# Kernel optimization log

Measured on AMD Instinct MI355X. Metric: run time of the kernel, lower is better.

The kernel has to match this reference:

```python
import jax, jax.numpy as jnp
import numpy as np

DIM = 1024
D_STATE = 16
D_CONV = 4
EXPAND = 2
D_INNER = DIM * EXPAND
DT_RANK = 64  # ceil(1024/16)
N_EXP = 8
TOP_K = 2
HID = DIM * 2
B, T = 2, 2048
EPS = 1e-5


def setup_inputs() -> dict:
    key = jax.random.key(0)
    ks = jax.random.split(key, 16)
    s = 0.02
    # dt bias init (softplus-inverse of dt in [1e-3, 1e-1]) as in the torch code
    dt_init = jnp.exp(jax.random.uniform(ks[0], (D_INNER,)) * (np.log(0.1) - np.log(0.001)) + np.log(0.001))
    dt_proj_b = dt_init + jnp.log(-jnp.expm1(-dt_init))
    A_log = jnp.broadcast_to(jnp.log(jnp.arange(1, D_STATE + 1, dtype=jnp.float32))[None, :], (D_INNER, D_STATE))
    return {
        "x": jax.random.normal(ks[1], (B, T, DIM), jnp.float32),
        "ssm_state": jnp.zeros((B, D_INNER, D_STATE), jnp.float32),
        "conv_state": jnp.zeros((B, D_INNER, D_CONV - 1), jnp.float32),
        "ln1_s": jnp.ones((DIM,), jnp.float32), "ln1_b": jnp.zeros((DIM,), jnp.float32),
        "ln2_s": jnp.ones((DIM,), jnp.float32), "ln2_b": jnp.zeros((DIM,), jnp.float32),
        "in_proj_w": jax.random.normal(ks[2], (2 * D_INNER, DIM), jnp.float32) * s,
        "conv_w": jax.random.normal(ks[3], (D_INNER, 1, D_CONV), jnp.float32) * 0.2,
        "conv_b": jnp.zeros((D_INNER,), jnp.float32),
        "x_proj_w": jax.random.normal(ks[4], (DT_RANK + 2 * D_STATE, D_INNER), jnp.float32) * s,
        "dt_proj_w": jax.random.normal(ks[5], (D_INNER, DT_RANK), jnp.float32) * s,
        "dt_proj_b": dt_proj_b,
        "A_log": A_log,
        "Dp": jnp.ones((D_INNER,), jnp.float32),
        "out_proj_w": jax.random.normal(ks[6], (DIM, D_INNER), jnp.float32) * s,
        "router_w": jax.random.normal(ks[7], (N_EXP, DIM), jnp.float32) * s,
        "w_gate": jax.random.normal(ks[8], (N_EXP, HID, DIM), jnp.float32) * s,
        "w_up": jax.random.normal(ks[9], (N_EXP, HID, DIM), jnp.float32) * s,
        "w_down": jax.random.normal(ks[10], (N_EXP, DIM, HID), jnp.float32) * s,
    }


def _layernorm(x, scale, bias):
    mu = x.mean(-1, keepdims=True)
    var = ((x - mu) ** 2).mean(-1, keepdims=True)
    return (x - mu) * jax.lax.rsqrt(var + EPS) * scale + bias


def _mamba(xn, ssm_state, conv_state, in_proj_w, conv_w, conv_b, x_proj_w, dt_proj_w, dt_proj_b, A_log, Dp, out_proj_w):
    xz = jnp.einsum("btd,ed->bte", xn, in_proj_w)          # [B,T,2*di]
    x_in, z = xz[..., :D_INNER], xz[..., D_INNER:]
    # causal depthwise conv with running buffer
    xc = jnp.concatenate([conv_state, x_in.transpose(0, 2, 1)], axis=2)  # [B,di,T+dc-1]
    new_conv_state = xc[:, :, -(D_CONV - 1):]
    conv = jax.lax.conv_general_dilated(xc, conv_w, (1,), "VALID",
                                        dimension_numbers=("NCH", "OIH", "NCH"),
                                        feature_group_count=D_INNER)
    conv = conv + conv_b[None, :, None]
    xcs = jax.nn.silu(conv).transpose(0, 2, 1)              # [B,T,di]
    proj = jnp.einsum("bti,pi->btp", xcs, x_proj_w)
    dt_raw = proj[..., :DT_RANK]
    Bp = proj[..., DT_RANK:DT_RANK + D_STATE]
    Cp = proj[..., DT_RANK + D_STATE:]
    dt = jax.nn.softplus(jnp.einsum("btr,ir->bti", dt_raw, dt_proj_w) + dt_proj_b)
    A = -jnp.exp(A_log)                                     # [di,ds]

    def step(h, inp):
        dt_t, B_t, C_t, x_t = inp                           # [B,di],[B,ds],[B,ds],[B,di]
        dA = jnp.exp(dt_t[..., None] * A)                   # [B,di,ds]
        dB = dt_t[..., None] * B_t[:, None, :]
        h = dA * h + dB * x_t[..., None]
        y = jnp.sum(h * C_t[:, None, :], -1) + Dp * x_t
        return h, y

    xs = (dt.transpose(1, 0, 2), Bp.transpose(1, 0, 2), Cp.transpose(1, 0, 2), xcs.transpose(1, 0, 2))
    h, ys = jax.lax.scan(step, ssm_state, xs)
    y = ys.transpose(1, 0, 2) * jax.nn.silu(z)
    out = jnp.einsum("bti,di->btd", y, out_proj_w)
    return out, h, new_conv_state


def _moe(x, router_w, w_gate, w_up, w_down):
    Bb, Tt, D = x.shape
    xf = x.reshape(-1, D)                                   # [N,D]
    probs = jax.nn.softmax(xf @ router_w.T, axis=-1)        # [N,E]
    tw, ti = jax.lax.top_k(probs, TOP_K)
    tw = tw / tw.sum(-1, keepdims=True)
    gate = jax.nn.silu(jnp.einsum("nd,ehd->neh", xf, w_gate))
    up = jnp.einsum("nd,ehd->neh", xf, w_up)
    eo = jnp.einsum("neh,edh->ned", gate * up, w_down)      # [N,E,D]
    sel = jnp.take_along_axis(eo, ti[:, :, None], axis=1)   # [N,K,D]
    out = (tw[..., None] * sel).sum(1)
    return out.reshape(Bb, Tt, D)


def reference(x, ssm_state, conv_state, ln1_s, ln1_b, ln2_s, ln2_b, in_proj_w, conv_w, conv_b,
              x_proj_w, dt_proj_w, dt_proj_b, A_log, Dp, out_proj_w, router_w, w_gate, w_up, w_down):
    mamba_out, h, new_conv = _mamba(_layernorm(x, ln1_s, ln1_b), ssm_state, conv_state,
                                    in_proj_w, conv_w, conv_b, x_proj_w, dt_proj_w, dt_proj_b,
                                    A_log, Dp, out_proj_w)
    x1 = x + mamba_out
    out = x1 + _moe(_layernorm(x1, ln2_s, ln2_b), router_w, w_gate, w_up, w_down)
    return out
```

## Files before the change

### kernel.cpp

```cpp
#include <hip/hip_runtime.h>
#include <hip/hip_bf16.h>
#include <math.h>

#define DIM 1024
#define D_STATE 16
#define D_CONV 4
#define D_INNER 2048
#define DT_RANK 64
#define N_EXP 8
#define TOP_K 2
#define HID 2048
#define BB 2
#define TT 2048
#define NTOK (BB*TT)
#define NSLOT (NTOK*TOP_K)
#define EPS 1e-5f
#define NCHUNK 64
#define CLEN (TT/NCHUNK)
#define XPJ_KS 8
#define XPJ_KLEN (D_INNER/XPJ_KS)

#define OFF_R0   ((size_t)0)
#define OFF_R1   ((size_t)4194304)
#define OFF_R2   ((size_t)8388608)
#define OFF_XZ   ((size_t)10485760)
#define OFF_H    OFF_XZ
#define OFF_WU   ((size_t)18874368)
#define OFF_XCS  ((size_t)27262976)
#define OFF_DTP  ((size_t)35651584)
#define OFF_X1   ((size_t)44040192)
#define OFF_PROJ ((size_t)48234496)
#define OFF_TW   ((size_t)48627712)
#define OFF_INT  ((size_t)48635904)
#define OFF_XPW  ((size_t)48668672)
#define IO_TI    0
#define IO_CNT   8192
#define IO_CUR   8200
#define IO_OFS   8208
#define IO_TOK   8216
#define IO_SLOT  16408

typedef __attribute__((ext_vector_type(4))) float f32x4;
typedef __attribute__((ext_vector_type(8))) __bf16 bf16x8;
typedef __attribute__((ext_vector_type(4))) __bf16 bf16x4;

__device__ __forceinline__ float siluf(float v){ return v / (1.f + expf(-v)); }

__device__ __forceinline__ f32x4 mfma16(bf16x8 a, bf16x8 b, f32x4 c){
    return __builtin_amdgcn_mfma_f32_16x16x32_bf16(a, b, c, 0, 0, 0);
}

__device__ __forceinline__ void gload16(const void* g, void* l){
    __builtin_amdgcn_global_load_lds(
        (const __attribute__((address_space(1))) unsigned int*)g,
        (__attribute__((address_space(3))) unsigned int*)l, 16, 0, 0);
}

__device__ __forceinline__ void cvt_store16(__bf16* dst, f32x4 a0, f32x4 a1, f32x4 a2, f32x4 a3){
    bf16x8 p0, p1;
    #pragma unroll
    for (int j = 0; j < 4; ++j){
        p0[j]   = (__bf16)a0[j];
        p0[j+4] = (__bf16)a1[j];
        p1[j]   = (__bf16)a2[j];
        p1[j+4] = (__bf16)a3[j];
    }
    *(bf16x8*)dst = p0;
    *(bf16x8*)(dst+8) = p1;
}

__global__ __launch_bounds__(256) void cvt_w_kernel(const float* __restrict__ src,
    __bf16* __restrict__ dst, int n4)
{
    int i = blockIdx.x*256 + threadIdx.x;
    int stride = gridDim.x*256;
    for (; i < n4; i += stride){
        f32x4 v = *(const f32x4*)(src + (size_t)i*4);
        bf16x4 o;
        o[0] = (__bf16)v[0]; o[1] = (__bf16)v[1];
        o[2] = (__bf16)v[2]; o[3] = (__bf16)v[3];
        *(bf16x4*)(dst + (size_t)i*4) = o;
    }
}

__global__ __launch_bounds__(256) void cvt_pad_xproj(const float* __restrict__ src,
    __bf16* __restrict__ dst)
{
    int i = blockIdx.x*256 + threadIdx.x;
    int base = i*4;
    int row = base >> 11;
    bf16x4 o;
    if (row < 96){
        f32x4 v = *(const f32x4*)(src + base);
        o[0] = (__bf16)v[0]; o[1] = (__bf16)v[1];
        o[2] = (__bf16)v[2]; o[3] = (__bf16)v[3];
    } else {
        o[0] = (__bf16)0.f; o[1] = (__bf16)0.f;
        o[2] = (__bf16)0.f; o[3] = (__bf16)0.f;
    }
    *(bf16x4*)(dst + base) = o;
}

__global__ __launch_bounds__(256) void ln_kernel(const float* __restrict__ x,
    const float* __restrict__ s, const float* __restrict__ b,
    __bf16* __restrict__ obf)
{
    int t = blockIdx.x;
    const float* xp = x + (size_t)t * DIM;
    float v[4]; float sum = 0.f, sq = 0.f;
    #pragma unroll
    for (int j = 0; j < 4; ++j){
        v[j] = xp[threadIdx.x + 256*j];
        sum += v[j]; sq += v[j]*v[j];
    }
    #pragma unroll
    for (int off = 32; off; off >>= 1){
        sum += __shfl_xor(sum, off, 64);
        sq  += __shfl_xor(sq , off, 64);
    }
    __shared__ float red[4][2];
    int w = threadIdx.x >> 6, lane = threadIdx.x & 63;
    if (lane == 0){ red[w][0] = sum; red[w][1] = sq; }
    __syncthreads();
    sum = red[0][0]+red[1][0]+red[2][0]+red[3][0];
    sq  = red[0][1]+red[1][1]+red[2][1]+red[3][1];
    float mu = sum * (1.f/DIM);
    float var = sq * (1.f/DIM) - mu*mu;
    float r = rsqrtf(var + EPS);
    #pragma unroll
    for (int j = 0; j < 4; ++j){
        int d = threadIdx.x + 256*j;
        obf[(size_t)t*DIM + d] = (__bf16)((v[j]-mu)*r*s[d] + b[d]);
    }
}

__global__ __launch_bounds__(256) void ln2_router_kernel(const float* __restrict__ x,
    const float* __restrict__ s, const float* __restrict__ b,
    const float* __restrict__ rw, __bf16* __restrict__ obf,
    float* __restrict__ tw, int* __restrict__ ti, int* __restrict__ counts)
{
    int t = blockIdx.x;
    const float* xp = x + (size_t)t * DIM;
    float v[4]; float sum = 0.f, sq = 0.f;
    #pragma unroll
    for (int j = 0; j < 4; ++j){
        v[j] = xp[threadIdx.x + 256*j];
        sum += v[j]; sq += v[j]*v[j];
    }
    #pragma unroll
    for (int off = 32; off; off >>= 1){
        sum += __shfl_xor(sum, off, 64);
        sq  += __shfl_xor(sq , off, 64);
    }
    __shared__ float red[4][2];
    __shared__ float red2[4][N_EXP];
    int w = threadIdx.x >> 6, lane = threadIdx.x & 63;
    if (lane == 0){ red[w][0] = sum; red[w][1] = sq; }
    __syncthreads();
    sum = red[0][0]+red[1][0]+red[2][0]+red[3][0];
    sq  = red[0][1]+red[1][1]+red[2][1]+red[3][1];
    float mu = sum * (1.f/DIM);
    float var = sq * (1.f/DIM) - mu*mu;
    float r = rsqrtf(var + EPS);
    float p[N_EXP] = {};
    #pragma unroll
    for (int j = 0; j < 4; ++j){
        int d = threadIdx.x + 256*j;
        float o = (v[j]-mu)*r*s[d] + b[d];
        obf[(size_t)t*DIM + d] = (__bf16)o;
        #pragma unroll
        for (int e = 0; e < N_EXP; ++e) p[e] += o * rw[e*DIM + d];
    }
    #pragma unroll
    for (int e = 0; e < N_EXP; ++e){
        #pragma unroll
        for (int off = 32; off; off >>= 1) p[e] += __shfl_xor(p[e], off, 64);
    }
    if (lane == 0){
        #pragma unroll
        for (int e = 0; e < N_EXP; ++e) red2[w][e] = p[e];
    }
    __syncthreads();
    if (threadIdx.x == 0){
        float q[N_EXP];
        #pragma unroll
        for (int e = 0; e < N_EXP; ++e)
            q[e] = red2[0][e]+red2[1][e]+red2[2][e]+red2[3][e];
        float mx = q[0];
        #pragma unroll
        for (int e = 1; e < N_EXP; ++e) mx = fmaxf(mx, q[e]);
        float ssum = 0.f;
        #pragma unroll
        for (int e = 0; e < N_EXP; ++e){ q[e] = expf(q[e]-mx); ssum += q[e]; }
        int i0 = 0;
        #pragma unroll
        for (int e = 1; e < N_EXP; ++e) if (q[e] > q[i0]) i0 = e;
        int i1 = (i0 == 0) ? 1 : 0;
        #pragma unroll
        for (int e = 0; e < N_EXP; ++e) if (e != i0 && q[e] > q[i1]) i1 = e;
        float w0 = q[i0]/ssum, w1 = q[i1]/ssum;
        float sw = w0 + w1; w0 /= sw; w1 /= sw;
        tw[t*2] = w0; tw[t*2+1] = w1;
        ti[t*2] = i0; ti[t*2+1] = i1;
        atomicAdd(&counts[i0], 1);
        atomicAdd(&counts[i1], 1);
    }
}

template<int MODE, int EPI, int CBF, int SWZ>
__global__ __launch_bounds__(256,3) void mfma_gemm_fast(
    const __bf16* __restrict__ A, const __bf16* __restrict__ W,
    const void* __restrict__ RG, void* __restrict__ Cv,
    const int* __restrict__ tok_of_slot, const int* __restrict__ counts,
    const int* __restrict__ offs, int M, int N, int K, int lda)
{
    int bx = blockIdx.x, by = blockIdx.y;
    if (SWZ){
        int nwg = gridDim.x*gridDim.y;
        int id = by*gridDim.x + bx;
        int swz = (id & 7)*(nwg >> 3) + (id >> 3);
        bx = swz % gridDim.x; by = swz / gridDim.x;
    }
    int e    = (MODE == 0) ? 0 : blockIdx.z;
    int cnt  = (MODE == 0) ? M : counts[e];
    int base = (MODE == 0) ? 0 : offs[e];
    int m0 = by * 128;
    if (m0 >= cnt) return;
    int n0 = bx * 128;
    const __bf16* We = W + (size_t)e * N * K;

    __shared__ __bf16 As[3*128*32];
    __shared__ __bf16 Ws[3*128*32];

    int tid = threadIdx.x;
    int wave = tid >> 6, lane = tid & 63;
    int c0 = wave*2, c1 = wave*2 + 1;
    int lr0 = c0*16 + (lane >> 2);
    int lr1 = c1*16 + (lane >> 2);
    int koff = (((lane & 3) ^ ((lane >> 3) & 3)) * 8);

    int ar0, ar1;
    {
        int m0c = m0 + lr0, m1c = m0 + lr1;
        if (MODE != 0){
            if (m0c >= cnt) m0c = cnt - 1;
            if (m1c >= cnt) m1c = cnt - 1;
        }
        if (MODE == 1){ ar0 = tok_of_slot[base + m0c]; ar1 = tok_of_slot[base + m1c]; }
        else if (MODE == 2){ ar0 = base + m0c; ar1 = base + m1c; }
        else { ar0 = m0c; ar1 = m1c; }
    }
    const __bf16* aS0 = A + (size_t)ar0 * lda + koff;
    const __bf16* aS1 = A + (size_t)ar1 * lda + koff;
    const __bf16* wS0 = We + (size_t)(n0 + lr0) * K + koff;
    const __bf16* wS1 = We + (size_t)(n0 + lr1) * K + koff;
    __bf16* ldsA0 = As + c0*512;
    __bf16* ldsA1 = As + c1*512;
    __bf16* ldsW0 = Ws + c0*512;
    __bf16* ldsW1 = Ws + c1*512;

    int wm = (wave >> 1) * 64, wn = (wave & 1) * 64;
    int fr = lane & 15;
    const int scb = (((lane >> 4) ^ ((lane >> 1) & 3)) * 8);

    f32x4 acc[4][4];
    #pragma unroll
    for (int i = 0; i < 4; ++i)
        #pragma unroll
        for (int j = 0; j < 4; ++j)
            acc[i][j] = (f32x4){0.f, 0.f, 0.f, 0.f};

    int NK = K >> 5;
    gload16(aS0, ldsA0);        gload16(aS1, ldsA1);
    gload16(wS0, ldsW0);        gload16(wS1, ldsW1);
    if (NK > 1){
        gload16(aS0 + 32, ldsA0 + 4096); gload16(aS1 + 32, ldsA1 + 4096);
        gload16(wS0 + 32, ldsW0 + 4096); gload16(wS1 + 32, ldsW1 + 4096);
    }

    int cur = 0;
    for (int t = 0; t < NK; ++t){
        if (t + 2 < NK){
            int nb = cur + 2; if (nb >= 3) nb -= 3;
            int off = nb*4096;
            size_t ko = (size_t)(t+2)*32;
            gload16(aS0 + ko, ldsA0 + off);
            gload16(aS1 + ko, ldsA1 + off);
            gload16(wS0 + ko, ldsW0 + off);
            gload16(wS1 + ko, ldsW1 + off);
            asm volatile("s_waitcnt vmcnt(8)" ::: "memory");
        } else if (t + 1 < NK){
            asm volatile("s_waitcnt vmcnt(4)" ::: "memory");
        } else {
            asm volatile("s_waitcnt vmcnt(0)" ::: "memory");
        }
        __builtin_amdgcn_s_barrier();
        int bo = cur*4096;
        bf16x8 af[4], bf[4];
        #pragma unroll
        for (int i = 0; i < 4; ++i)
            af[i] = *(const bf16x8*)&As[bo + (wm + i*16 + fr)*32 + scb];
        #pragma unroll
        for (int j = 0; j < 4; ++j)
            bf[j] = *(const bf16x8*)&Ws[bo + (wn + j*16 + fr)*32 + scb];
        __builtin_amdgcn_s_setprio(1);
        #pragma unroll
        for (int i = 0; i < 4; ++i)
            #pragma unroll
            for (int j = 0; j < 4; ++j)
                acc[i][j] = mfma16(af[i], bf[j], acc[i][j]);
        __builtin_amdgcn_s_setprio(0);
        __builtin_amdgcn_s_barrier();
        cur = cur + 1; if (cur >= 3) cur -= 3;
    }

    int orow = (lane >> 4) * 4;
    int ocol = lane & 15;
    #pragma unroll
    for (int i = 0; i < 4; ++i){
        #pragma unroll
        for (int jj = 0; jj < 4; ++jj){
            #pragma unroll
            for (int j = 0; j < 4; ++j){
                int m = m0 + wm + i*16 + orow + j;
                int n = n0 + wn + jj*16 + ocol;
                if (m < cnt){
                    size_t row = (size_t)(base + m);
                    float v = acc[i][jj][j];
                    if (EPI == 1) v += ((const float*)RG)[row * (size_t)N + n];
                    if (CBF) ((__bf16*)Cv)[row * (size_t)N + n] = (__bf16)v;
                    else     ((float* )Cv)[row * (size_t)N + n] = v;
                }
            }
        }
    }
}

__global__ __launch_bounds__(256,2) void moe_gateup_fast(
    const __bf16* __restrict__ A, const __bf16* __restrict__ Wg,
    const __bf16* __restrict__ Wu, const int* __restrict__ tok_of_slot,
    const int* __restrict__ counts, const int* __restrict__ offs,
    __bf16* __restrict__ H)
{
    int e = blockIdx.z;
    int cnt = counts[e];
    int base = offs[e];
    int m0 = blockIdx.y * 128;
    if (m0 >= cnt) return;
    int n0 = blockIdx.x * 128;
    const __bf16* Wge = Wg + (size_t)e * HID * DIM;
    const __bf16* Wue = Wu + (size_t)e * HID * DIM;

    __shared__ __bf16 As[3*128*32];
    __shared__ __bf16 Gs[3*128*32];
    __shared__ __bf16 Us[3*128*32];

    int tid = threadIdx.x;
    int wave = tid >> 6, lane = tid & 63;
    int c0 = wave*2, c1 = wave*2 + 1;
    int lr0 = c0*16 + (lane >> 2);
    int lr1 = c1*16 + (lane >> 2);
    int koff = (((lane & 3) ^ ((lane >> 3) & 3)) * 8);

    int m0c = m0 + lr0, m1c = m0 + lr1;
    if (m0c >= cnt) m0c = cnt - 1;
    if (m1c >= cnt) m1c = cnt - 1;
    int ar0 = tok_of_slot[base + m0c];
    int ar1 = tok_of_slot[base + m1c];

    const __bf16* aS0 = A + (size_t)ar0 * DIM + koff;
    const __bf16* aS1 = A + (size_t)ar1 * DIM + koff;
    const __bf16* gS0 = Wge + (size_t)(n0 + lr0) * DIM + koff;
    const __bf16* gS1 = Wge + (size_t)(n0 + lr1) * DIM + koff;
    const __bf16* uS0 = Wue + (size_t)(n0 + lr0) * DIM + koff;
    const __bf16* uS1 = Wue + (size_t)(n0 + lr1) * DIM + koff;
    __bf16* ldsA0 = As + c0*512;
    __bf16* ldsA1 = As + c1*512;
    __bf16* ldsG0 = Gs + c0*512;
    __bf16* ldsG1 = Gs + c1*512;
    __bf16* ldsU0 = Us + c0*512;
    __bf16* ldsU1 = Us + c1*512;

    int wm = (wave >> 1) * 64, wn = (wave & 1) * 64;
    int fr = lane & 15;
    const int scb = (((lane >> 4) ^ ((lane >> 1) & 3)) * 8);

    f32x4 accg[4][4], accu[4][4];
    #pragma unroll
    for (int i = 0; i < 4; ++i)
        #pragma unroll
        for (int j = 0; j < 4; ++j){
            accg[i][j] = (f32x4){0.f, 0.f, 0.f, 0.f};
            accu[i][j] = (f32x4){0.f, 0.f, 0.f, 0.f};
        }

    gload16(aS0, ldsA0); gload16(aS1, ldsA1);
    gload16(gS0, ldsG0); gload16(gS1, ldsG1);
    gload16(uS0, ldsU0); gload16(uS1, ldsU1);
    gload16(aS0 + 32, ldsA0 + 4096); gload16(aS1 + 32, ldsA1 + 4096);
    gload16(gS0 + 32, ldsG0 + 4096); gload16(gS1 + 32, ldsG1 + 4096);
    gload16(uS0 + 32, ldsU0 + 4096); gload16(uS1 + 32, ldsU1 + 4096);

    const int NK = DIM >> 5;
    int cur = 0;
    for (int t = 0; t < NK; ++t){
        if (t + 2 < NK){
            int nb = cur + 2; if (nb >= 3) nb -= 3;
            int off = nb*4096;
            size_t ko = (size_t)(t+2)*32;
            gload16(aS0 + ko, ldsA0 + off);
            gload16(aS1 + ko, ldsA1 + off);
            gload16(gS0 + ko, ldsG0 + off);
            gload16(gS1 + ko, ldsG1 + off);
            gload16(uS0 + ko, ldsU0 + off);
            gload16(uS1 + ko, ldsU1 + off);
            asm volatile("s_waitcnt vmcnt(12)" ::: "memory");
        } else if (t + 1 < NK){
            asm volatile("s_waitcnt vmcnt(6)" ::: "memory");
        } else {
            asm volatile("s_waitcnt vmcnt(0)" ::: "memory");
        }
        __builtin_amdgcn_s_barrier();
        int bo = cur*4096;
        bf16x8 af[4], gf[4], uf[4];
        #pragma unroll
        for (int i = 0; i < 4; ++i){
            af[i] = *(const bf16x8*)&As[bo + (wm + i*16 + fr)*32 + scb];
            gf[i] = *(const bf16x8*)&Gs[bo + (wn + i*16 + fr)*32 + scb];
            uf[i] = *(const bf16x8*)&Us[bo + (wn + i*16 + fr)*32 + scb];
        }
        __builtin_amdgcn_s_setprio(1);
        #pragma unroll
        for (int i = 0; i < 4; ++i)
            #pragma unroll
            for (int j = 0; j < 4; ++j){
                accg[i][j] = mfma16(af[i], gf[j], accg[i][j]);
                accu[i][j] = mfma16(af[i], uf[j], accu[i][j]);
            }
        __builtin_amdgcn_s_setprio(0);
        __builtin_amdgcn_s_barrier();
        cur = cur + 1; if (cur >= 3) cur -= 3;
    }

    int orow = (lane >> 4) * 4;
    int ocol = lane & 15;
    #pragma unroll
    for (int i = 0; i < 4; ++i){
        #pragma unroll
        for (int jj = 0; jj < 4; ++jj){
            #pragma unroll
            for (int j = 0; j < 4; ++j){
                int m = m0 + wm + i*16 + orow + j;
                if (m < cnt){
                    int n = n0 + wn + jj*16 + ocol;
                    size_t row = (size_t)(base + m);
                    float g = accg[i][jj][j], u = accu[i][jj][j];
                    H[row * (size_t)HID + n] = (__bf16)(siluf(g) * u);
                }
            }
        }
    }
}

__global__ __launch_bounds__(256,3) void xproj_ks_kernel(
    const __bf16* __restrict__ A, const __bf16* __restrict__ W,
    float* __restrict__ Cpart)
{
    int m0 = blockIdx.y * 128;
    int kbeg = blockIdx.z * XPJ_KLEN;

    __shared__ __bf16 As[3*128*32];
    __shared__ __bf16 Ws[3*128*32];

    int tid = threadIdx.x;
    int wave = tid >> 6, lane = tid & 63;
    int c0 = wave*2, c1 = wave*2 + 1;
    int lr0 = c0*16 + (lane >> 2);
    int lr1 = c1*16 + (lane >> 2);
    int koff = (((lane & 3) ^ ((lane >> 3) & 3)) * 8);

    const __bf16* aS0 = A + (size_t)(m0 + lr0) * D_INNER + kbeg + koff;
    const __bf16* aS1 = A + (size_t)(m0 + lr1) * D_INNER + kbeg + koff;
    const __bf16* wS0 = W + (size_t)lr0 * D_INNER + kbeg + koff;
    const __bf16* wS1 = W + (size_t)lr1 * D_INNER + kbeg + koff;
    __bf16* ldsA0 = As + c0*512;
    __bf16* ldsA1 = As + c1*512;
    __bf16* ldsW0 = Ws + c0*512;
    __bf16* ldsW1 = Ws + c1*512;

    int wm = (wave >> 1) * 64, wn = (wave & 1) * 64;
    int fr = lane & 15;
    const int scb = (((lane >> 4) ^ ((lane >> 1) & 3)) * 8);

    f32x4 acc[4][4];
    #pragma unroll
    for (int i = 0; i < 4; ++i)
        #pragma unroll
        for (int j = 0; j < 4; ++j)
            acc[i][j] = (f32x4){0.f, 0.f, 0.f, 0.f};

    gload16(aS0, ldsA0); gload16(aS1, ldsA1);
    gload16(wS0, ldsW0); gload16(wS1, ldsW1);
    gload16(aS0 + 32, ldsA0 + 4096); gload16(aS1 + 32, ldsA1 + 4096);
    gload16(wS0 + 32, ldsW0 + 4096); gload16(wS1 + 32, ldsW1 + 4096);

    const int NK = XPJ_KLEN >> 5;
    int cur = 0;
    for (int t = 0; t < NK; ++t){
        if (t + 2 < NK){
            int nb = cur + 2; if (nb >= 3) nb -= 3;
            int off = nb*4096;
            size_t ko = (size_t)(t+2)*32;
            gload16(aS0 + ko, ldsA0 + off);
            gload16(aS1 + ko, ldsA1 + off);
            gload16(wS0 + ko, ldsW0 + off);
            gload16(wS1 + ko, ldsW1 + off);
            asm volatile("s_waitcnt vmcnt(8)" ::: "memory");
        } else if (t + 1 < NK){
            asm volatile("s_waitcnt vmcnt(4)" ::: "memory");
        } else {
            asm volatile("s_waitcnt vmcnt(0)" ::: "memory");
        }
        __builtin_amdgcn_s_barrier();
        int bo = cur*4096;
        bf16x8 af[4], bf[4];
        #pragma unroll
        for (int i = 0; i < 4; ++i)
            af[i] = *(const bf16x8*)&As[bo + (wm + i*16 + fr)*32 + scb];
        #pragma unroll
        for (int j = 0; j < 4; ++j)
            bf[j] = *(const bf16x8*)&Ws[bo + (wn + j*16 + fr)*32 + scb];
        __builtin_amdgcn_s_setprio(1);
        #pragma unroll
        for (int i = 0; i < 4; ++i)
            #pragma unroll
            for (int j = 0; j < 4; ++j)
                acc[i][j] = mfma16(af[i], bf[j], acc[i][j]);
        __builtin_amdgcn_s_setprio(0);
        __builtin_amdgcn_s_barrier();
        cur = cur + 1; if (cur >= 3) cur -= 3;
    }

    float* Cz = Cpart + (size_t)blockIdx.z * NTOK * 128;
    int orow = (lane >> 4) * 4;
    int ocol = lane & 15;
    #pragma unroll
    for (int i = 0; i < 4; ++i){
        #pragma unroll
        for (int jj = 0; jj < 4; ++jj){
            #pragma unroll
            for (int j = 0; j < 4; ++j){
                int m = m0 + wm + i*16 + orow + j;
                int n = wn + jj*16 + ocol;
                Cz[(size_t)m * 128 + n] = acc[i][jj][j];
            }
        }
    }
}

__global__ __launch_bounds__(256) void xproj_reduce(const float* __restrict__ Cpart,
    float* __restrict__ proj)
{
    int idx = blockIdx.x*256 + threadIdx.x;
    int t = idx / 96, n = idx - t*96;
    float s = 0.f;
    #pragma unroll
    for (int z = 0; z < XPJ_KS; ++z)
        s += Cpart[(size_t)z * NTOK * 128 + (size_t)t * 128 + n];
    proj[idx] = s;
}

__global__ __launch_bounds__(256,2) void dt_gemm(
    const float* __restrict__ A, const float* __restrict__ W,
    const float* __restrict__ bias, float* __restrict__ C,
    int M, int N, int K, int lda)
{
    int m0 = blockIdx.y * 128;
    int n0 = blockIdx.x * 128;

    __shared__ __bf16 As[128*32];
    __shared__ __bf16 Ws[128*32];

    int tid = threadIdx.x;
    int srow = tid >> 1;
    int scol = (tid & 1) * 16;

    const float* af = A + (size_t)(m0 + srow) * lda + scol;
    const float* wptr = W + (size_t)(n0 + srow) * K + scol;

    f32x4 raf[4], rw[4];
    #pragma unroll
    for (int q = 0; q < 4; ++q){
        raf[q] = *(const f32x4*)(af + q*4);
        rw[q]  = *(const f32x4*)(wptr + q*4);
    }

    int wave = tid >> 6, lane = tid & 63;
    int wm = (wave >> 1) * 64, wn = (wave & 1) * 64;
    int fr = lane & 15, fk = (lane >> 4) * 8;

    f32x4 acc[4][4];
    #pragma unroll
    for (int i = 0; i < 4; ++i)
        #pragma unroll
        for (int j = 0; j < 4; ++j)
            acc[i][j] = (f32x4){0.f, 0.f, 0.f, 0.f};

    for (int k0 = 0; k0 < K; k0 += 32){
        cvt_store16(&As[srow*32 + scol], raf[0], raf[1], raf[2], raf[3]);
        cvt_store16(&Ws[srow*32 + scol], rw[0], rw[1], rw[2], rw[3]);
        __syncthreads();
        if (k0 + 32 < K){
            #pragma unroll
            for (int q = 0; q < 4; ++q){
                raf[q] = *(const f32x4*)(af + k0 + 32 + q*4);
                rw[q]  = *(const f32x4*)(wptr + k0 + 32 + q*4);
            }
        }
        bf16x8 afr[4], bfr[4];
        #pragma unroll
        for (int i = 0; i < 4; ++i)
            afr[i] = *(const bf16x8*)&As[(wm + i*16 + fr)*32 + fk];
        #pragma unroll
        for (int i = 0; i < 4; ++i)
            bfr[i] = *(const bf16x8*)&Ws[(wn + i*16 + fr)*32 + fk];
        #pragma unroll
        for (int i = 0; i < 4; ++i)
            #pragma unroll
            for (int j = 0; j < 4; ++j)
                acc[i][j] = mfma16(afr[i], bfr[j], acc[i][j]);
        __syncthreads();
    }

    int orow = (lane >> 4) * 4;
    int ocol = lane & 15;
    #pragma unroll
    for (int i = 0; i < 4; ++i){
        #pragma unroll
        for (int jj = 0; jj < 4; ++jj){
            #pragma unroll
            for (int j = 0; j < 4; ++j){
                int m = m0 + wm + i*16 + orow + j;
                int n = n0 + wn + jj*16 + ocol;
                if (m < M && n < N){
                    float v = acc[i][jj][j] + bias[n];
                    v = (v > 20.f) ? v : log1pf(expf(v));
                    C[(size_t)m * N + n] = v;
                }
            }
        }
    }
}

__global__ __launch_bounds__(256) void conv_kernel(const float* __restrict__ xz,
    const float* __restrict__ cs, const float* __restrict__ cw,
    const float* __restrict__ cb, float* __restrict__ xcs,
    __bf16* __restrict__ xcs_bf)
{
    int idx = blockIdx.x*256 + threadIdx.x;
    int d = idx & (D_INNER-1);
    int bt = idx >> 11;
    int b = bt >> 11;
    int t = bt & (TT-1);
    float acc = cb[d];
    #pragma unroll
    for (int k = 0; k < 4; ++k){
        int tau = t + k - 3;
        float xv;
        if (tau >= 0) xv = xz[(size_t)(b*TT + tau)*(2*D_INNER) + d];
        else          xv = cs[((size_t)b*D_INNER + d)*3 + (tau + 3)];
        acc += cw[d*4 + k] * xv;
    }
    float v = siluf(acc);
    xcs[idx] = v;
    xcs_bf[idx] = (__bf16)v;
}

__global__ __launch_bounds__(256) void scan_pass1(const float* __restrict__ dtp,
    const float* __restrict__ proj, const float* __restrict__ xcs,
    const float* __restrict__ A_log, float* __restrict__ hend,
    float* __restrict__ sumdt)
{
    int gid = blockIdx.x*256 + threadIdx.x;
    int bd = gid & (BB*D_INNER-1);
    int chunk = gid >> 12;
    int b = bd >> 11, d = bd & (D_INNER-1);
    float As[D_STATE], h[D_STATE];
    #pragma unroll
    for (int s = 0; s < D_STATE; ++s){
        As[s] = -__expf(A_log[d*D_STATE + s]);
        h[s] = 0.f;
    }
    float sdt = 0.f;
    int base = b*TT + chunk*CLEN;
    for (int t = 0; t < CLEN; ++t){
        size_t bt = (size_t)(base + t);
        float dt = dtp[bt*D_INNER + d];
        float x  = xcs[bt*D_INNER + d];
        f32x4 Bv[4];
        #pragma unroll
        for (int q = 0; q < 4; ++q) Bv[q] = *(const f32x4*)(proj + bt*96 + DT_RANK + q*4);
        float dtx = dt * x;
        sdt += dt;
        #pragma unroll
        for (int s = 0; s < D_STATE; ++s)
            h[s] = __expf(dt*As[s])*h[s] + Bv[s>>2][s&3]*dtx;
    }
    size_t hb = ((size_t)bd*NCHUNK + chunk)*D_STATE;
    #pragma unroll
    for (int q = 0; q < 4; ++q)
        *(f32x4*)(hend + hb + q*4) = (f32x4){h[q*4], h[q*4+1], h[q*4+2], h[q*4+3]};
    sumdt[bd*NCHUNK + chunk] = sdt;
}

__global__ __launch_bounds__(256) void scan_combine(const float* __restrict__ hend,
    const float* __restrict__ sumdt, const float* __restrict__ A_log,
    const float* __restrict__ ssm0, float* __restrict__ hstart)
{
    int gid = blockIdx.x*256 + threadIdx.x;
    int s = gid & 15;
    int bd = gid >> 4;
    int b = bd >> 11, d = bd & (D_INNER-1);
    float As = -__expf(A_log[d*D_STATE + s]);
    float h = ssm0[((size_t)b*D_INNER + d)*D_STATE + s];
    for (int c = 0; c < NCHUNK; ++c){
        size_t idx = ((size_t)bd*NCHUNK + c)*D_STATE + s;
        hstart[idx] = h;
        h = hend[idx] + __expf(As * sumdt[bd*NCHUNK + c]) * h;
    }
}

__global__ __launch_bounds__(256) void scan_pass3(const float* __restrict__ dtp,
    const float* __restrict__ proj, const float* __restrict__ xcs,
    const float* __restrict__ xz, const float* __restrict__ A_log,
    const float* __restrict__ Dp, const float* __restrict__ hstart,
    __bf16* __restrict__ ym)
{
    int gid = blockIdx.x*256 + threadIdx.x;
    int bd = gid & (BB*D_INNER-1);
    int chunk = gid >> 12;
    int b = bd >> 11, d = bd & (D_INNER-1);
    float As[D_STATE], h[D_STATE];
    #pragma unroll
    for (int s = 0; s < D_STATE; ++s)
        As[s] = -__expf(A_log[d*D_STATE + s]);
    size_t hb = ((size_t)bd*NCHUNK + chunk)*D_STATE;
    #pragma unroll
    for (int q = 0; q < 4; ++q){
        f32x4 hv = *(const f32x4*)(hstart + hb + q*4);
        h[q*4] = hv[0]; h[q*4+1] = hv[1]; h[q*4+2] = hv[2]; h[q*4+3] = hv[3];
    }
    float Dd = Dp[d];
    int base = b*TT + chunk*CLEN;
    for (int t = 0; t < CLEN; ++t){
        size_t bt = (size_t)(base + t);
        float dt = dtp[bt*D_INNER + d];
        float x  = xcs[bt*D_INNER + d];
        f32x4 Bv[4], Cv[4];
        #pragma unroll
        for (int q = 0; q < 4; ++q){
            Bv[q] = *(const f32x4*)(proj + bt*96 + DT_RANK + q*4);
            Cv[q] = *(const f32x4*)(proj + bt*96 + DT_RANK + D_STATE + q*4);
        }
        float dtx = dt * x;
        float p = 0.f;
        #pragma unroll
        for (int s = 0; s < D_STATE; ++s){
            h[s] = __expf(dt*As[s])*h[s] + Bv[s>>2][s&3]*dtx;
            p += h[s] * Cv[s>>2][s&3];
        }
        float y = p + Dd*x;
        float z = xz[bt*(2*D_INNER) + D_INNER + d];
        float sz = z / (1.f + __expf(-z));
        ym[bt*D_INNER + d] = (__bf16)(y * sz);
    }
}

__global__ void offs_kernel(const int* __restrict__ counts, int* __restrict__ offs)
{
    if (threadIdx.x == 0 && blockIdx.x == 0){
        int s = 0;
        for (int e = 0; e < N_EXP; ++e){ offs[e] = s; s += counts[e]; }
    }
}

__global__ __launch_bounds__(256) void assign_kernel(const int* __restrict__ ti,
    const int* __restrict__ offs, int* __restrict__ cursors,
    int* __restrict__ tok_of_slot, int* __restrict__ slot_of)
{
    int t = blockIdx.x*256 + threadIdx.x;
    if (t >= NTOK) return;
    #pragma unroll
    for (int k = 0; k < TOP_K; ++k){
        int e = ti[t*2 + k];
        int pos = atomicAdd(&cursors[e], 1);
        int slot = offs[e] + pos;
        tok_of_slot[slot] = t;
        slot_of[t*2 + k] = slot;
    }
}

__global__ __launch_bounds__(256) void final_kernel(const float* __restrict__ x1,
    const float* __restrict__ down_out, const float* __restrict__ tw,
    const int* __restrict__ slot_of, float* __restrict__ out)
{
    int idx4 = blockIdx.x*256 + threadIdx.x;
    int t = idx4 >> 8;
    int c = idx4 & 255;
    float w0 = tw[t*2], w1 = tw[t*2+1];
    size_t s0 = (size_t)slot_of[t*2] * DIM;
    size_t s1 = (size_t)slot_of[t*2+1] * DIM;
    float4 a = *(const float4*)(x1 + (size_t)t*DIM + c*4);
    float4 d0 = *(const float4*)(down_out + s0 + c*4);
    float4 d1 = *(const float4*)(down_out + s1 + c*4);
    float4 r;
    r.x = a.x + w0*d0.x + w1*d1.x;
    r.y = a.y + w0*d0.y + w1*d1.y;
    r.z = a.z + w0*d0.z + w1*d1.z;
    r.w = a.w + w0*d0.w + w1*d1.w;
    *(float4*)(out + (size_t)t*DIM + c*4) = r;
}

extern "C" void kernel_launch(void* const* d_in, const int* in_sizes, int n_in,
                              void* d_out, int out_size, void* d_ws, size_t ws_size,
                              hipStream_t stream)
{
    const float* x        = (const float*)d_in[0];
    const float* ssm0     = (const float*)d_in[1];
    const float* conv0    = (const float*)d_in[2];
    const float* ln1_s    = (const float*)d_in[3];
    const float* ln1_b    = (const float*)d_in[4];
    const float* ln2_s    = (const float*)d_in[5];
    const float* ln2_b    = (const float*)d_in[6];
    const float* in_proj  = (const float*)d_in[7];
    const float* conv_w   = (const float*)d_in[8];
    const float* conv_b   = (const float*)d_in[9];
    const float* x_proj   = (const float*)d_in[10];
    const float* dt_proj  = (const float*)d_in[11];
    const float* dt_b     = (const float*)d_in[12];
    const float* A_log    = (const float*)d_in[13];
    const float* Dp       = (const float*)d_in[14];
    const float* out_proj = (const float*)d_in[15];
    const float* router_w = (const float*)d_in[16];
    const float* w_gate   = (const float*)d_in[17];
    const float* w_up     = (const float*)d_in[18];
    const float* w_down   = (const float*)d_in[19];
    float* out = (float*)d_out;

    float* ws = (float*)d_ws;
    __bf16* xn_bf  = (__bf16*)(ws + OFF_R0);
    float*  hend   = ws + OFF_R0;
    __bf16* ym_bf  = (__bf16*)(ws + OFF_R0);
    float*  xpart  = ws + OFF_R1;
    float*  hst    = ws + OFF_R1;
    float*  sdt    = ws + OFF_R2;
    __bf16* opbf   = (__bf16*)(ws + OFF_R2);
    __bf16* xn2bf  = (__bf16*)(ws + OFF_R2);
    float*  xz     = ws + OFF_XZ;
    __bf16* H      = (__bf16*)(ws + OFF_H);
    __bf16* wubf   = (__bf16*)(ws + OFF_WU);
    float*  xcs    = ws + OFF_XCS;
    float*  dnout  = ws + OFF_XCS;
    float*  dtp    = ws + OFF_DTP;
    __bf16* ipbf   = (__bf16*)(ws + OFF_DTP);
    __bf16* wgbf   = (__bf16*)(ws + OFF_DTP);
    __bf16* wdbf   = (__bf16*)(ws + OFF_DTP);
    __bf16* xcs_bf = (__bf16*)(ws + OFF_X1);
    float*  x1     = ws + OFF_X1;
    float*  proj   = ws + OFF_PROJ;
    float*  tw     = ws + OFF_TW;
    __bf16* xpw    = (__bf16*)(ws + OFF_XPW);
    int*    ip     = (int*)(ws + OFF_INT);
    int* ti          = ip + IO_TI;
    int* counts      = ip + IO_CNT;
    int* cursors     = ip + IO_CUR;
    int* offs        = ip + IO_OFS;
    int* tok_of_slot = ip + IO_TOK;
    int* slot_of     = ip + IO_SLOT;

    hipMemsetAsync(counts, 0, 16*sizeof(int), stream);

    cvt_w_kernel<<<1024, 256, 0, stream>>>(in_proj, ipbf, (2*D_INNER*DIM)/4);
    ln_kernel<<<NTOK, 256, 0, stream>>>(x, ln1_s, ln1_b, xn_bf);
    mfma_gemm_fast<0,0,0,1><<<dim3(32,32), 256, 0, stream>>>(xn_bf, ipbf, nullptr, xz,
        nullptr, nullptr, nullptr, NTOK, 2*D_INNER, DIM, DIM);
    conv_kernel<<<(NTOK*D_INNER)/256, 256, 0, stream>>>(xz, conv0, conv_w, conv_b, xcs, xcs_bf);
    cvt_pad_xproj<<<256, 256, 0, stream>>>(x_proj, xpw);
    xproj_ks_kernel<<<dim3(1,32,XPJ_KS), 256, 0, stream>>>(xcs_bf, xpw, xpart);
    xproj_reduce<<<(NTOK*96)/256, 256, 0, stream>>>(xpart, proj);
    dt_gemm<<<dim3(16,32), 256, 0, stream>>>(proj, dt_proj, dt_b, dtp,
        NTOK, D_INNER, DT_RANK, 96);
    scan_pass1<<<1024, 256, 0, stream>>>(dtp, proj, xcs, A_log, hend, sdt);
    scan_combine<<<256, 256, 0, stream>>>(hend, sdt, A_log, ssm0, hst);
    scan_pass3<<<1024, 256, 0, stream>>>(dtp, proj, xcs, xz, A_log, Dp, hst, ym_bf);
    cvt_w_kernel<<<512, 256, 0, stream>>>(out_proj, opbf, (DIM*D_INNER)/4);
    mfma_gemm_fast<0,1,0,1><<<dim3(8,32), 256, 0, stream>>>(ym_bf, opbf, x, x1,
        nullptr, nullptr, nullptr, NTOK, DIM, D_INNER, D_INNER);
    ln2_router_kernel<<<NTOK, 256, 0, stream>>>(x1, ln2_s, ln2_b, router_w,
        xn2bf, tw, ti, counts);
    offs_kernel<<<1, 64, 0, stream>>>(counts, offs);
    assign_kernel<<<NTOK/256, 256, 0, stream>>>(ti, offs, cursors, tok_of_slot, slot_of);
    cvt_w_kernel<<<2048, 256, 0, stream>>>(w_gate, wgbf, (N_EXP*HID*DIM)/4);
    cvt_w_kernel<<<2048, 256, 0, stream>>>(w_up, wubf, (N_EXP*HID*DIM)/4);
    moe_gateup_fast<<<dim3(HID/128, 64, N_EXP), 256, 0, stream>>>(xn2bf, wgbf, wubf,
        tok_of_slot, counts, offs, H);
    cvt_w_kernel<<<2048, 256, 0, stream>>>(w_down, wdbf, (N_EXP*DIM*HID)/4);
    mfma_gemm_fast<2,0,0,0><<<dim3(DIM/128, 64, N_EXP), 256, 0, stream>>>(H, wdbf, nullptr, dnout,
        tok_of_slot, counts, offs, NSLOT, DIM, HID, HID);
    final_kernel<<<(NTOK*DIM/4)/256, 256, 0, stream>>>(x1, dnout, tw, slot_of, out);
}
```

Before: 738.5 us.

## Retile MoE gate/up GEMM to 64-row tiles with persistent M loop

The MoE gate/up kernel moves from a 128x128 tile with triple buffering to a 64x128 tile with double buffering. Each block now loops over M-tiles with stride gridDim.y instead of returning early. Launch bounds go to 3 waves per SIMD and grid.y is halved, with the aim of raising occupancy and cutting wasted work on the ragged last tile per expert. In exchange each A-row tile reuses less weight data and there is one fewer prefetch stage to hide load latency.

Result: no change. 732.5 us (-0.8%).

```diff
diff --git a/kernel.cpp b/kernel.cpp
--- a/kernel.cpp
+++ b/kernel.cpp
@@ -336,7 +336,7 @@
     }
 }
 
-__global__ __launch_bounds__(256,2) void moe_gateup_fast(
+__global__ __launch_bounds__(256,3) void moe_gateup_fast(
     const __bf16* __restrict__ A, const __bf16* __restrict__ Wg,
     const __bf16* __restrict__ Wu, const int* __restrict__ tok_of_slot,
     const int* __restrict__ counts, const int* __restrict__ offs,
@@ -345,117 +345,103 @@
     int e = blockIdx.z;
     int cnt = counts[e];
     int base = offs[e];
-    int m0 = blockIdx.y * 128;
-    if (m0 >= cnt) return;
     int n0 = blockIdx.x * 128;
     const __bf16* Wge = Wg + (size_t)e * HID * DIM;
     const __bf16* Wue = Wu + (size_t)e * HID * DIM;
 
-    __shared__ __bf16 As[3*128*32];
-    __shared__ __bf16 Gs[3*128*32];
-    __shared__ __bf16 Us[3*128*32];
+    __shared__ __bf16 As[2*64*32];
+    __shared__ __bf16 Gs[2*128*32];
+    __shared__ __bf16 Us[2*128*32];
 
     int tid = threadIdx.x;
     int wave = tid >> 6, lane = tid & 63;
-    int c0 = wave*2, c1 = wave*2 + 1;
-    int lr0 = c0*16 + (lane >> 2);
-    int lr1 = c1*16 + (lane >> 2);
+    int lrow = lane >> 2;
     int koff = (((lane & 3) ^ ((lane >> 3) & 3)) * 8);
 
-    int m0c = m0 + lr0, m1c = m0 + lr1;
-    if (m0c >= cnt) m0c = cnt - 1;
-    if (m1c >= cnt) m1c = cnt - 1;
-    int ar0 = tok_of_slot[base + m0c];
-    int ar1 = tok_of_slot[base + m1c];
-
-    const __bf16* aS0 = A + (size_t)ar0 * DIM + koff;
-    const __bf16* aS1 = A + (size_t)ar1 * DIM + koff;
-    const __bf16* gS0 = Wge + (size_t)(n0 + lr0) * DIM + koff;
-    const __bf16* gS1 = Wge + (size_t)(n0 + lr1) * DIM + koff;
-    const __bf16* uS0 = Wue + (size_t)(n0 + lr0) * DIM + koff;
-    const __bf16* uS1 = Wue + (size_t)(n0 + lr1) * DIM + koff;
-    __bf16* ldsA0 = As + c0*512;
-    __bf16* ldsA1 = As + c1*512;
-    __bf16* ldsG0 = Gs + c0*512;
-    __bf16* ldsG1 = Gs + c1*512;
-    __bf16* ldsU0 = Us + c0*512;
-    __bf16* ldsU1 = Us + c1*512;
-
-    int wm = (wave >> 1) * 64, wn = (wave & 1) * 64;
+    const __bf16* gS0 = Wge + (size_t)(n0 + wave*32      + lrow) * DIM + koff;
+    const __bf16* gS1 = Wge + (size_t)(n0 + wave*32 + 16 + lrow) * DIM + koff;
+    const __bf16* uS0 = Wue + (size_t)(n0 + wave*32      + lrow) * DIM + koff;
+    const __bf16* uS1 = Wue + (size_t)(n0 + wave*32 + 16 + lrow) * DIM + koff;
+    __bf16* ldsA  = As + wave*512;
+    __bf16* ldsG0 = Gs + (wave*2    )*512;
+    __bf16* ldsG1 = Gs + (wave*2 + 1)*512;
+    __bf16* ldsU0 = Us + (wave*2    )*512;
+    __bf16* ldsU1 = Us + (wave*2 + 1)*512;
+
     int fr = lane & 15;
     const int scb = (((lane >> 4) ^ ((lane >> 1) & 3)) * 8);
-
-    f32x4 accg[4][4], accu[4][4];
-    #pragma unroll
-    for (int i = 0; i < 4; ++i)
-        #pragma unroll
-        for (int j = 0; j < 4; ++j){
-            accg[i][j] = (f32x4){0.f, 0.f, 0.f, 0.f};
-            accu[i][j] = (f32x4){0.f, 0.f, 0.f, 0.f};
-        }
-
-    gload16(aS0, ldsA0); gload16(aS1, ldsA1);
-    gload16(gS0, ldsG0); gload16(gS1, ldsG1);
-    gload16(uS0, ldsU0); gload16(uS1, ldsU1);
-    gload16(aS0 + 32, ldsA0 + 4096); gload16(aS1 + 32, ldsA1 + 4096);
-    gload16(gS0 + 32, ldsG0 + 4096); gload16(gS1 + 32, ldsG1 + 4096);
-    gload16(uS0 + 32, ldsU0 + 4096); gload16(uS1 + 32, ldsU1 + 4096);
-
-    const int NK = DIM >> 5;
-    int cur = 0;
-    for (int t = 0; t < NK; ++t){
-        if (t + 2 < NK){
-            int nb = cur + 2; if (nb >= 3) nb -= 3;
-            int off = nb*4096;
-            size_t ko = (size_t)(t+2)*32;
-            gload16(aS0 + ko, ldsA0 + off);
-            gload16(aS1 + ko, ldsA1 + off);
-            gload16(gS0 + ko, ldsG0 + off);
-            gload16(gS1 + ko, ldsG1 + off);
-            gload16(uS0 + ko, ldsU0 + off);
-            gload16(uS1 + ko, ldsU1 + off);
-            asm volatile("s_waitcnt vmcnt(12)" ::: "memory");
-        } else if (t + 1 < NK){
-            asm volatile("s_waitcnt vmcnt(6)" ::: "memory");
-        } else {
-            asm volatile("s_waitcnt vmcnt(0)" ::: "memory");
-        }
-        __builtin_amdgcn_s_barrier();
-        int bo = cur*4096;
-        bf16x8 af[4], gf[4], uf[4];
-        #pragma unroll
-        for (int i = 0; i < 4; ++i){
-            af[i] = *(const bf16x8*)&As[bo + (wm + i*16 + fr)*32 + scb];
-            gf[i] = *(const bf16x8*)&Gs[bo + (wn + i*16 + fr)*32 + scb];
-            uf[i] = *(const bf16x8*)&Us[bo + (wn + i*16 + fr)*32 + scb];
-        }
-        __builtin_amdgcn_s_setprio(1);
-        #pragma unroll
-        for (int i = 0; i < 4; ++i)
-            #pragma unroll
-            for (int j = 0; j < 4; ++j){
-                accg[i][j] = mfma16(af[i], gf[j], accg[i][j]);
-                accu[i][j] = mfma16(af[i], uf[j], accu[i][j]);
-            }
-        __builtin_amdgcn_s_setprio(0);
-        __builtin_amdgcn_s_barrier();
-        cur = cur + 1; if (cur >= 3) cur -= 3;
-    }
-
     int orow = (lane >> 4) * 4;
     int ocol = lane & 15;
-    #pragma unroll
-    for (int i = 0; i < 4; ++i){
-        #pragma unroll
-        for (int jj = 0; jj < 4; ++jj){
-            #pragma unroll
-            for (int j = 0; j < 4; ++j){
-                int m = m0 + wm + i*16 + orow + j;
-                if (m < cnt){
-                    int n = n0 + wn + jj*16 + ocol;
-                    size_t row = (size_t)(base + m);
-                    float g = accg[i][jj][j], u = accu[i][jj][j];
-                    H[row * (size_t)HID + n] = (__bf16)(siluf(g) * u);
+    const int NK = DIM >> 5;
+
+    for (int mb = blockIdx.y; mb * 64 < cnt; mb += gridDim.y){
+        int m0 = mb * 64;
+        int mc = m0 + wave*16 + lrow;
+        if (mc >= cnt) mc = cnt - 1;
+        const __bf16* aS = A + (size_t)tok_of_slot[base + mc] * DIM + koff;
+
+        f32x4 accg[4][2], accu[4][2];
+        #pragma unroll
+        for (int i = 0; i < 4; ++i)
+            #pragma unroll
+            for (int j = 0; j < 2; ++j){
+                accg[i][j] = (f32x4){0.f, 0.f, 0.f, 0.f};
+                accu[i][j] = (f32x4){0.f, 0.f, 0.f, 0.f};
+            }
+
+        gload16(aS, ldsA);
+        gload16(gS0, ldsG0); gload16(gS1, ldsG1);
+        gload16(uS0, ldsU0); gload16(uS1, ldsU1);
+
+        int bo = 0;
+        for (int t = 0; t < NK; ++t){
+            if (t + 1 < NK){
+                int nA = (bo ^ 1) * 2048, nW = (bo ^ 1) * 4096;
+                size_t ko = (size_t)(t+1)*32;
+                gload16(aS + ko, ldsA + nA);
+                gload16(gS0 + ko, ldsG0 + nW); gload16(gS1 + ko, ldsG1 + nW);
+                gload16(uS0 + ko, ldsU0 + nW); gload16(uS1 + ko, ldsU1 + nW);
+                asm volatile("s_waitcnt vmcnt(5)" ::: "memory");
+            } else {
+                asm volatile("s_waitcnt vmcnt(0)" ::: "memory");
+            }
+            __builtin_amdgcn_s_barrier();
+            int boA = bo*2048, boW = bo*4096;
+            bf16x8 af[4], gf[2], uf[2];
+            #pragma unroll
+            for (int i = 0; i < 4; ++i)
+                af[i] = *(const bf16x8*)&As[boA + (i*16 + fr)*32 + scb];
+            #pragma unroll
+            for (int j = 0; j < 2; ++j){
+                gf[j] = *(const bf16x8*)&Gs[boW + (wave*32 + j*16 + fr)*32 + scb];
+                uf[j] = *(const bf16x8*)&Us[boW + (wave*32 + j*16 + fr)*32 + scb];
+            }
+            __builtin_amdgcn_s_setprio(1);
+            #pragma unroll
+            for (int i = 0; i < 4; ++i)
+                #pragma unroll
+                for (int j = 0; j < 2; ++j){
+                    accg[i][j] = mfma16(af[i], gf[j], accg[i][j]);
+                    accu[i][j] = mfma16(af[i], uf[j], accu[i][j]);
+                }
+            __builtin_amdgcn_s_setprio(0);
+            __builtin_amdgcn_s_barrier();
+            bo ^= 1;
+        }
+
+        #pragma unroll
+        for (int i = 0; i < 4; ++i){
+            #pragma unroll
+            for (int j = 0; j < 2; ++j){
+                #pragma unroll
+                for (int j4 = 0; j4 < 4; ++j4){
+                    int m = m0 + i*16 + orow + j4;
+                    if (m < cnt){
+                        size_t row = (size_t)(base + m);
+                        int n = n0 + wave*32 + j*16 + ocol;
+                        float g = accg[i][j][j4], u = accu[i][j][j4];
+                        H[row * (size_t)HID + n] = (__bf16)(siluf(g) * u);
+                    }
                 }
             }
         }
@@ -902,7 +888,7 @@
     assign_kernel<<<NTOK/256, 256, 0, stream>>>(ti, offs, cursors, tok_of_slot, slot_of);
     cvt_w_kernel<<<2048, 256, 0, stream>>>(w_gate, wgbf, (N_EXP*HID*DIM)/4);
     cvt_w_kernel<<<2048, 256, 0, stream>>>(w_up, wubf, (N_EXP*HID*DIM)/4);
-    moe_gateup_fast<<<dim3(HID/128, 64, N_EXP), 256, 0, stream>>>(xn2bf, wgbf, wubf,
+    moe_gateup_fast<<<dim3(HID/128, 32, N_EXP), 256, 0, stream>>>(xn2bf, wgbf, wubf,
         tok_of_slot, counts, offs, H);
     cvt_w_kernel<<<2048, 256, 0, stream>>>(w_down, wdbf, (N_EXP*DIM*HID)/4);
     mfma_gemm_fast<2,0,0,0><<<dim3(DIM/128, 64, N_EXP), 256, 0, stream>>>(H, wdbf, nullptr, dnout,
```
